# Kernel tuning notes

Measured on AMD Instinct MI355X. Metric: run time of the kernel, lower is better.

## Reference

```python
import jax, jax.numpy as jnp
import numpy as np

B, S, E, H = 4, 2048, 1024, 16
D = E // H  # head_dim = 64


def setup_inputs() -> dict:
    key = jax.random.key(0)
    ks = jax.random.split(key, 5)
    return {
        "hidden_states": jax.random.normal(ks[0], (B, S, E), dtype=jnp.float32),
        "c_attn_w": jax.random.normal(ks[1], (E, 3 * E), dtype=jnp.float32) * 0.02,
        "c_attn_b": jax.random.normal(ks[2], (3 * E,), dtype=jnp.float32) * 0.02,
        "c_proj_w": jax.random.normal(ks[3], (E, E), dtype=jnp.float32) * 0.02,
        "c_proj_b": jax.random.normal(ks[4], (E,), dtype=jnp.float32) * 0.02,
    }


def reference(hidden_states, c_attn_w, c_attn_b, c_proj_w, c_proj_b):
    b, s, e = hidden_states.shape
    # Conv1D c_attn: y = x @ W + b  -> qkv [b, s, 3E]
    qkv = hidden_states @ c_attn_w + c_attn_b
    q, k, v = jnp.split(qkv, 3, axis=-1)
    # split heads -> [b, H, s, D]
    def split_heads(t):
        return t.reshape(b, s, H, D).transpose(0, 2, 1, 3)
    q, k, v = split_heads(q), split_heads(k), split_heads(v)
    # QK^T scaled by sqrt(head_dim)
    scores = jnp.einsum("bhqd,bhkd->bhqk", q, k) / jnp.sqrt(
        jnp.asarray(D, dtype=q.dtype)
    )
    # causal mask (tril), masked positions get dtype min
    causal = jnp.tril(jnp.ones((s, s), dtype=bool))[None, None]
    mask_value = jnp.finfo(scores.dtype).min
    scores = jnp.where(causal, scores, mask_value)
    attn = jax.nn.softmax(scores, axis=-1)
    # attend to values, merge heads
    out = jnp.einsum("bhqk,bhkd->bhqd", attn, v)
    out = out.transpose(0, 2, 1, 3).reshape(b, s, e)
    # Conv1D c_proj
    return out @ c_proj_w + c_proj_b
```

## Files before the change

kernel.cpp:

```cpp
#include <hip/hip_runtime.h>
#include <hip/hip_bf16.h>
#include <cstdint>
#include <cstddef>

#define BB 4
#define SS 2048
#define EE 1024
#define HH 16
#define DD 64

typedef __attribute__((ext_vector_type(8))) short bf16x8;
typedef __attribute__((ext_vector_type(4))) float f32x4;

__device__ __forceinline__ short f2bf(float f) {
    union { float f; uint32_t u; } x; x.f = f;
    uint32_t r = (x.u + 0x7fffu + ((x.u >> 16) & 1u)) >> 16;
    return (short)r;
}
__device__ __forceinline__ short f2bf_fast(float f) {
    union { float f; uint32_t u; } x; x.f = f;
    return (short)((x.u + 0x8000u) >> 16);
}

__device__ __forceinline__ void gload16(const void* g, void* l) {
    __builtin_amdgcn_global_load_lds(
        (__attribute__((address_space(1))) uint32_t*)(uintptr_t)g,
        (__attribute__((address_space(3))) uint32_t*)(uint32_t)(uintptr_t)l,
        16, 0, 0);
}

#define WAIT_BARRIER(N)                                          \
    asm volatile("s_waitcnt vmcnt(" #N ")" ::: "memory");        \
    __builtin_amdgcn_s_barrier();                                \
    __builtin_amdgcn_sched_barrier(0);

template<int CTRL>
__device__ __forceinline__ float dppmove(float v) {
    return __int_as_float(__builtin_amdgcn_update_dpp(
        0, __float_as_int(v), CTRL, 0xf, 0xf, true));
}
#define ROW_REDUCE(vals, OP)                                             \
    _Pragma("unroll") for (int _r = 0; _r < 4; ++_r) {                   \
        vals[_r] = OP(vals[_r], dppmove<0xB1>(vals[_r]));                \
        vals[_r] = OP(vals[_r], dppmove<0x4E>(vals[_r]));                \
        vals[_r] = OP(vals[_r], dppmove<0x124>(vals[_r]));               \
        vals[_r] = OP(vals[_r], dppmove<0x128>(vals[_r]));               \
    }
__device__ __forceinline__ float opmax(float a, float b) { return fmaxf(a, b); }
__device__ __forceinline__ float opsum(float a, float b) { return a + b; }

__global__ void cast_kernel(const float* __restrict__ in, short* __restrict__ out, int n4) {
    int stride = gridDim.x * blockDim.x;
    for (int i = blockIdx.x * blockDim.x + threadIdx.x; i < n4; i += stride) {
        float4 v = reinterpret_cast<const float4*>(in)[i];
        short4 o;
        o.x = f2bf(v.x); o.y = f2bf(v.y); o.z = f2bf(v.z); o.w = f2bf(v.w);
        reinterpret_cast<short4*>(out)[i] = o;
    }
}

__global__ void transpose_cast_kernel(const float* __restrict__ in, short* __restrict__ out,
                                      int ncols, int nrows) {
    __shared__ float ts[32][33];
    const int t = threadIdx.x;
    const int r = t >> 3, c4 = (t & 7) * 4;
    const int n0 = blockIdx.x * 32, k0 = blockIdx.y * 32;
    float4 v = *reinterpret_cast<const float4*>(&in[(size_t)(k0 + r) * ncols + n0 + c4]);
    ts[c4 + 0][r] = v.x; ts[c4 + 1][r] = v.y; ts[c4 + 2][r] = v.z; ts[c4 + 3][r] = v.w;
    __syncthreads();
    short4 ov;
    ov.x = f2bf(ts[r][c4 + 0]); ov.y = f2bf(ts[r][c4 + 1]);
    ov.z = f2bf(ts[r][c4 + 2]); ov.w = f2bf(ts[r][c4 + 3]);
    *reinterpret_cast<short4*>(&out[(size_t)(n0 + r) * nrows + k0 + c4]) = ov;
}

__global__ __launch_bounds__(512, 2)
void gemm_qkv(const short* __restrict__ A, const short* __restrict__ Bt,
              const float* __restrict__ bias,
              short* __restrict__ Qo, short* __restrict__ Ko, short* __restrict__ Vo)
{
    __shared__ short As[3][4096];
    __shared__ short Bs[3][8192];
    const int tid  = threadIdx.x;
    const int lane = tid & 63, wid = tid >> 6;
    const int wr = wid >> 2, wc = wid & 3;
    const int l15 = lane & 15, lhi = lane >> 4;
    const int m0 = blockIdx.y * 128, n0 = blockIdx.x * 256;
    const int sr   = lane >> 2;
    const int scol = 8 * ((lane & 3) ^ ((lane >> 3) & 3));
    const int rdx  = (lhi ^ ((l15 >> 1) & 3)) << 4;

    f32x4 acc[4][4] = {};

#define QKV_STAGE(tt, bufi)                                                      \
    {                                                                            \
        const int kk = (tt) * 32;                                                \
        gload16(&A[(size_t)(m0 + wid * 16 + sr) * EE + kk + scol],               \
                (char*)&As[bufi][0] + wid * 1024);                               \
        gload16(&Bt[(size_t)(n0 + wid * 32 + sr) * EE + kk + scol],              \
                (char*)&Bs[bufi][0] + wid * 2048);                               \
        gload16(&Bt[(size_t)(n0 + wid * 32 + 16 + sr) * EE + kk + scol],         \
                (char*)&Bs[bufi][0] + wid * 2048 + 1024);                        \
    }

    QKV_STAGE(0, 0)
    QKV_STAGE(1, 1)
    WAIT_BARRIER(3)

    for (int kt = 0; kt < 32; ++kt) {
        const int cur = kt % 3;
        if (kt + 2 < 32) { const int nb = (kt + 2) % 3; QKV_STAGE(kt + 2, nb) }

        bf16x8 af[4], bfr[4];
        #pragma unroll
        for (int mm = 0; mm < 4; ++mm)
            af[mm] = *reinterpret_cast<const bf16x8*>(
                (const char*)&As[cur][0] + (wr * 64 + mm * 16 + l15) * 64 + rdx);
        #pragma unroll
        for (int nn = 0; nn < 4; ++nn)
            bfr[nn] = *reinterpret_cast<const bf16x8*>(
                (const char*)&Bs[cur][0] + (wc * 64 + nn * 16 + l15) * 64 + rdx);
        #pragma unroll
        for (int mm = 0; mm < 4; ++mm)
            #pragma unroll
            for (int nn = 0; nn < 4; ++nn)
                acc[mm][nn] = __builtin_amdgcn_mfma_f32_16x16x32_bf16(af[mm], bfr[nn], acc[mm][nn], 0, 0, 0);

        if (kt < 30)       { WAIT_BARRIER(3) }
        else if (kt == 30) { WAIT_BARRIER(0) }
    }
#undef QKV_STAGE

    const int part = n0 >> 10;
    #pragma unroll
    for (int mm = 0; mm < 4; ++mm) {
        #pragma unroll
        for (int nn = 0; nn < 4; ++nn) {
            const int gcol = n0 + wc * 64 + nn * 16 + l15;
            const float bv = bias[gcol];
            const int e = gcol & 1023;
            const int h = e >> 6, d = e & 63;
            const int grow0 = m0 + wr * 64 + mm * 16 + lhi * 4;
            const int bidx = grow0 >> 11;
            const int s0 = grow0 & 2047;
            const int bh = bidx * HH + h;
            if (part == 2) {
                short4 pk;
                pk.x = f2bf(acc[mm][nn][0] + bv);
                pk.y = f2bf(acc[mm][nn][1] + bv);
                pk.z = f2bf(acc[mm][nn][2] + bv);
                pk.w = f2bf(acc[mm][nn][3] + bv);
                *reinterpret_cast<short4*>(&Vo[((size_t)bh * DD + d) * SS + s0]) = pk;
            } else if (part == 0) {
                #pragma unroll
                for (int r = 0; r < 4; ++r)
                    Qo[((size_t)bh * SS + s0 + r) * DD + d] = f2bf((acc[mm][nn][r] + bv) * 0.18033688f);
            } else {
                #pragma unroll
                for (int r = 0; r < 4; ++r)
                    Ko[((size_t)bh * SS + s0 + r) * DD + d] = f2bf(acc[mm][nn][r] + bv);
            }
        }
    }
}

__global__ __launch_bounds__(256, 2)
void gemm_proj(const short* __restrict__ A, const short* __restrict__ Bt,
               const float* __restrict__ bias, float* __restrict__ Co)
{
    __shared__ short As[3][4096];
    __shared__ short Bs[3][4096];
    const int tid  = threadIdx.x;
    const int lane = tid & 63, wid = tid >> 6;
    const int wr = wid >> 1, wc = wid & 1;
    const int l15 = lane & 15, lhi = lane >> 4;
    const int m0 = blockIdx.y * 128, n0 = blockIdx.x * 128;
    const int sr   = lane >> 2;
    const int scol = 8 * ((lane & 3) ^ ((lane >> 3) & 3));
    const int rdx  = (lhi ^ ((l15 >> 1) & 3)) << 4;

    f32x4 acc[4][4] = {};

#define PROJ_STAGE(tt, bufi)                                                     \
    {                                                                            \
        const int kk = (tt) * 32;                                                \
        _Pragma("unroll")                                                        \
        for (int p = 0; p < 2; ++p) {                                            \
            const int c = wid * 2 + p;                                           \
            gload16(&A [(size_t)(m0 + c * 16 + sr) * EE + kk + scol],            \
                    (char*)&As[bufi][0] + c * 1024);                             \
            gload16(&Bt[(size_t)(n0 + c * 16 + sr) * EE + kk + scol],            \
                    (char*)&Bs[bufi][0] + c * 1024);                             \
        }                                                                        \
    }

    PROJ_STAGE(0, 0)
    PROJ_STAGE(1, 1)
    WAIT_BARRIER(4)

    for (int kt = 0; kt < 32; ++kt) {
        const int cur = kt % 3;
        if (kt + 2 < 32) { const int nb = (kt + 2) % 3; PROJ_STAGE(kt + 2, nb) }

        bf16x8 af[4], bfr[4];
        #pragma unroll
        for (int mm = 0; mm < 4; ++mm)
            af[mm] = *reinterpret_cast<const bf16x8*>(
                (const char*)&As[cur][0] + (wr * 64 + mm * 16 + l15) * 64 + rdx);
        #pragma unroll
        for (int nn = 0; nn < 4; ++nn)
            bfr[nn] = *reinterpret_cast<const bf16x8*>(
                (const char*)&Bs[cur][0] + (wc * 64 + nn * 16 + l15) * 64 + rdx);
        #pragma unroll
        for (int mm = 0; mm < 4; ++mm)
            #pragma unroll
            for (int nn = 0; nn < 4; ++nn)
                acc[mm][nn] = __builtin_amdgcn_mfma_f32_16x16x32_bf16(af[mm], bfr[nn], acc[mm][nn], 0, 0, 0);

        if (kt < 30)       { WAIT_BARRIER(4) }
        else if (kt == 30) { WAIT_BARRIER(0) }
    }
#undef PROJ_STAGE

    #pragma unroll
    for (int mm = 0; mm < 4; ++mm) {
        #pragma unroll
        for (int nn = 0; nn < 4; ++nn) {
            const int gcol = n0 + wc * 64 + nn * 16 + l15;
            const float bv = bias[gcol];
            #pragma unroll
            for (int r = 0; r < 4; ++r) {
                const int grow = m0 + wr * 64 + mm * 16 + lhi * 4 + r;
                Co[(size_t)grow * EE + gcol] = acc[mm][nn][r] + bv;
            }
        }
    }
}

__global__ __launch_bounds__(256, 4)
void attn_kernel(const short* __restrict__ Q, const short* __restrict__ K,
                 const short* __restrict__ Vt, short* __restrict__ CTX)
{
    __shared__ short Ks[4096];
    __shared__ short Vs[2][4096];
    __shared__ short Ps[4][1024];
    const int tid  = threadIdx.x;
    const int lane = tid & 63, wid = tid >> 6;
    const int l15 = lane & 15, lhi = lane >> 4;
    const int bid  = blockIdx.x;
    const int bh   = (bid & 7) * 8 + ((bid >> 3) & 7);
    const int pair = bid >> 6;
    const int b = bh >> 4, h = bh & 15;
    const size_t base = (size_t)bh * (SS * DD);
    const short* VtBase = Vt + (size_t)bh * (DD * SS);
    char* const pw = (char*)&Ps[wid][0];

    const int srow = lane >> 3;
    const int scol = 8 * ((lane & 7) ^ srow);

    for (int phase = 0; phase < 2; ++phase) {
        const int t = phase ? (31 - pair) : pair;
        const int q0 = t * 64;
        const int qbase = q0 + wid * 16;

        bf16x8 qa[2];
        qa[0] = *reinterpret_cast<const bf16x8*>(&Q[base + (size_t)(qbase + l15) * DD + lhi * 8]);
        qa[1] = *reinterpret_cast<const bf16x8*>(&Q[base + (size_t)(qbase + l15) * DD + 32 + lhi * 8]);

        f32x4 o[4] = {};
        float lrow[4] = {0.f, 0.f, 0.f, 0.f};

        #pragma unroll
        for (int p = 0; p < 2; ++p) {
            const int c = wid * 2 + p;
            gload16(&K     [base + (size_t)(c * 8 + srow) * DD + scol], (char*)Ks + c * 1024);
            gload16(&VtBase[(size_t)(c * 8 + srow) * SS + scol],        (char*)&Vs[0][0] + c * 1024);
        }
        __syncthreads();

        for (int kt = 0; kt <= t; ++kt) {
            const int cur = kt & 1;

            f32x4 sc[4];
            #pragma unroll
            for (int n = 0; n < 4; ++n) {
                const int row = n * 16 + l15;
                f32x4 cacc = {};
                #pragma unroll
                for (int ks = 0; ks < 2; ++ks) {
                    const int byteoff = (ks * 64 + lhi * 16) ^ ((l15 & 7) << 4);
                    bf16x8 kb = *reinterpret_cast<const bf16x8*>((const char*)Ks + row * 128 + byteoff);
                    cacc = __builtin_amdgcn_mfma_f32_16x16x32_bf16(qa[ks], kb, cacc, 0, 0, 0);
                }
                sc[n] = cacc;
            }

            __syncthreads();

            if (kt < t) {
                const int k1 = (kt + 1) * 64;
                #pragma unroll
                for (int p = 0; p < 2; ++p) {
                    const int c = wid * 2 + p;
                    gload16(&K     [base + (size_t)(k1 + c * 8 + srow) * DD + scol], (char*)Ks + c * 1024);
                    gload16(&VtBase[(size_t)(c * 8 + srow) * SS + k1 + scol], (char*)&Vs[cur ^ 1][0] + c * 1024);
                }
            }

            if (kt == t) {
                #pragma unroll
                for (int n = 0; n < 4; ++n) {
                    const int col = n * 16 + l15;
                    #pragma unroll
                    for (int r = 0; r < 4; ++r) {
                        const int qrow = wid * 16 + lhi * 4 + r;
                        if (col > qrow) sc[n][r] = -1e30f;
                    }
                }
            }
            #pragma unroll
            for (int n = 0; n < 4; ++n)
                #pragma unroll
                for (int r = 0; r < 4; ++r) sc[n][r] = __builtin_amdgcn_exp2f(sc[n][r]);
            #pragma unroll
            for (int n = 0; n < 4; ++n)
                #pragma unroll
                for (int r = 0; r < 4; ++r) {
                    const int q = lhi * 4 + r;
                    const int cb = (n * 32 + l15 * 2) ^ ((q & 7) << 4);
                    *reinterpret_cast<short*>(pw + q * 128 + cb) = f2bf_fast(sc[n][r]);
                }
            bf16x8 pa[2];
            #pragma unroll
            for (int ks = 0; ks < 2; ++ks)
                pa[ks] = *reinterpret_cast<const bf16x8*>(
                    pw + l15 * 128 + ((ks * 64 + lhi * 16) ^ ((l15 & 7) << 4)));
            #pragma unroll
            for (int dg = 0; dg < 4; ++dg) {
                const int row = dg * 16 + l15;
                #pragma unroll
                for (int ks = 0; ks < 2; ++ks) {
                    const int byteoff = (ks * 64 + lhi * 16) ^ ((l15 & 7) << 4);
                    bf16x8 vb = *reinterpret_cast<const bf16x8*>((const char*)&Vs[cur][0] + row * 128 + byteoff);
                    o[dg] = __builtin_amdgcn_mfma_f32_16x16x32_bf16(pa[ks], vb, o[dg], 0, 0, 0);
                }
            }
            float tsum[4];
            #pragma unroll
            for (int r = 0; r < 4; ++r)
                tsum[r] = (sc[0][r] + sc[1][r]) + (sc[2][r] + sc[3][r]);
            ROW_REDUCE(tsum, opsum)
            #pragma unroll
            for (int r = 0; r < 4; ++r) lrow[r] += tsum[r];

            __syncthreads();
        }

        #pragma unroll
        for (int dg = 0; dg < 4; ++dg)
            #pragma unroll
            for (int r = 0; r < 4; ++r) {
                int s = qbase + lhi * 4 + r;
                float val = o[dg][r] / lrow[r];
                CTX[(size_t)(b * SS + s) * EE + h * DD + dg * 16 + l15] = f2bf(val);
            }
    }
}

extern "C" void kernel_launch(void* const* d_in, const int* in_sizes, int n_in,
                              void* d_out, int out_size, void* d_ws, size_t ws_size,
                              hipStream_t stream) {
    const float* hs     = (const float*)d_in[0];
    const float* attn_w = (const float*)d_in[1];
    const float* attn_b = (const float*)d_in[2];
    const float* proj_w = (const float*)d_in[3];
    const float* proj_b = (const float*)d_in[4];
    float* out = (float*)d_out;

    char* ws = (char*)d_ws;
    short* Xb    = (short*)(ws + 0);
    short* WqkvT = (short*)(ws + 16777216);
    short* WprojT= (short*)(ws + 23068672);
    short* Qb    = (short*)(ws + 25165824);
    short* Kb    = (short*)(ws + 41943040);
    short* Vb    = (short*)(ws + 58720256);
    short* CTX   = Xb;

    cast_kernel<<<dim3(2048), dim3(256), 0, stream>>>(hs, Xb, (BB * SS * EE) / 4);
    transpose_cast_kernel<<<dim3(3 * EE / 32, EE / 32), dim3(256), 0, stream>>>(attn_w, WqkvT, 3 * EE, EE);
    transpose_cast_kernel<<<dim3(EE / 32, EE / 32), dim3(256), 0, stream>>>(proj_w, WprojT, EE, EE);

    gemm_qkv<<<dim3(3 * EE / 256, BB * SS / 128), dim3(512), 0, stream>>>(
        Xb, WqkvT, attn_b, Qb, Kb, Vb);

    attn_kernel<<<dim3(1024), dim3(256), 0, stream>>>(Qb, Kb, Vb, CTX);

    gemm_proj<<<dim3(EE / 128, BB * SS / 128), dim3(256), 0, stream>>>(
        CTX, WprojT, proj_b, out);
}
```

Before: 169.5 us.

## Rewrite QKV GEMM as 256x256 tile with 8-phase ping-pong pipeline

The QKV projection GEMM moves from a 128x256 tile with a K=32 triple buffer to a 256x256 tile with K=64 double-buffered chunks. Each iteration interleaves LDS fragment reads, the async global-to-LDS loads and MFMA groups across eight barrier-separated phases, and raises wave priority around the MFMA groups. The aim is more data reuse per tile and better overlap of loads with matrix math. In exchange it needs more accumulator registers (occupancy drops to 1 block per CU) and launches half as many blocks, which may leave CUs underused; the projection GEMM only gets its variables renamed.

```diff
diff --git a/kernel.cpp b/kernel.cpp
--- a/kernel.cpp
+++ b/kernel.cpp
@@ -28,11 +28,6 @@
         (__attribute__((address_space(3))) uint32_t*)(uint32_t)(uintptr_t)l,
         16, 0, 0);
 }
-
-#define WAIT_BARRIER(N)                                          \
-    asm volatile("s_waitcnt vmcnt(" #N ")" ::: "memory");        \
-    __builtin_amdgcn_s_barrier();                                \
-    __builtin_amdgcn_sched_barrier(0);
 
 template<int CTRL>
 __device__ __forceinline__ float dppmove(float v) {
@@ -74,73 +69,90 @@
     *reinterpret_cast<short4*>(&out[(size_t)(n0 + r) * nrows + k0 + c4]) = ov;
 }
 
-__global__ __launch_bounds__(512, 2)
+__global__ __launch_bounds__(512, 1)
 void gemm_qkv(const short* __restrict__ A, const short* __restrict__ Bt,
               const float* __restrict__ bias,
               short* __restrict__ Qo, short* __restrict__ Ko, short* __restrict__ Vo)
 {
-    __shared__ short As[3][4096];
-    __shared__ short Bs[3][8192];
+    __shared__ short As[2][4][4096];
+    __shared__ short Bs[2][4][4096];
     const int tid  = threadIdx.x;
     const int lane = tid & 63, wid = tid >> 6;
     const int wr = wid >> 2, wc = wid & 3;
     const int l15 = lane & 15, lhi = lane >> 4;
-    const int m0 = blockIdx.y * 128, n0 = blockIdx.x * 256;
-    const int sr   = lane >> 2;
-    const int scol = 8 * ((lane & 3) ^ ((lane >> 3) & 3));
-    const int rdx  = (lhi ^ ((l15 >> 1) & 3)) << 4;
-
-    f32x4 acc[4][4] = {};
-
-#define QKV_STAGE(tt, bufi)                                                      \
-    {                                                                            \
-        const int kk = (tt) * 32;                                                \
-        gload16(&A[(size_t)(m0 + wid * 16 + sr) * EE + kk + scol],               \
-                (char*)&As[bufi][0] + wid * 1024);                               \
-        gload16(&Bt[(size_t)(n0 + wid * 32 + sr) * EE + kk + scol],              \
-                (char*)&Bs[bufi][0] + wid * 2048);                               \
-        gload16(&Bt[(size_t)(n0 + wid * 32 + 16 + sr) * EE + kk + scol],         \
-                (char*)&Bs[bufi][0] + wid * 2048 + 1024);                        \
-    }
-
-    QKV_STAGE(0, 0)
-    QKV_STAGE(1, 1)
-    WAIT_BARRIER(3)
-
-    for (int kt = 0; kt < 32; ++kt) {
-        const int cur = kt % 3;
-        if (kt + 2 < 32) { const int nb = (kt + 2) % 3; QKV_STAGE(kt + 2, nb) }
-
-        bf16x8 af[4], bfr[4];
-        #pragma unroll
-        for (int mm = 0; mm < 4; ++mm)
-            af[mm] = *reinterpret_cast<const bf16x8*>(
-                (const char*)&As[cur][0] + (wr * 64 + mm * 16 + l15) * 64 + rdx);
-        #pragma unroll
-        for (int nn = 0; nn < 4; ++nn)
-            bfr[nn] = *reinterpret_cast<const bf16x8*>(
-                (const char*)&Bs[cur][0] + (wc * 64 + nn * 16 + l15) * 64 + rdx);
-        #pragma unroll
-        for (int mm = 0; mm < 4; ++mm)
-            #pragma unroll
-            for (int nn = 0; nn < 4; ++nn)
-                acc[mm][nn] = __builtin_amdgcn_mfma_f32_16x16x32_bf16(af[mm], bfr[nn], acc[mm][nn], 0, 0, 0);
-
-        if (kt < 30)       { WAIT_BARRIER(3) }
-        else if (kt == 30) { WAIT_BARRIER(0) }
-    }
-#undef QKV_STAGE
+    const int m0 = blockIdx.y * 256, n0 = blockIdx.x * 256;
+    const int srow = lane >> 3;
+    const int scol = 8 * ((lane & 7) ^ srow);
+    const int xorr = (l15 & 7) << 4;
+
+    f32x4 acc[8][4] = {};
+    bf16x8 af[4][2];
+    bf16x8 bfr[2][2][2];
+
+#define STGA(p, c0, c1, tt)                                                              \
+    gload16(&A[(size_t)(m0 + (c0)*64 + wid*8 + srow) * EE + (tt)*64 + scol],             \
+            (char*)&As[p][c0][0] + wid*1024);                                            \
+    gload16(&A[(size_t)(m0 + (c1)*64 + wid*8 + srow) * EE + (tt)*64 + scol],             \
+            (char*)&As[p][c1][0] + wid*1024);
+#define STGB(p, c0, c1, tt)                                                              \
+    gload16(&Bt[(size_t)(n0 + (c0)*64 + wid*8 + srow) * EE + (tt)*64 + scol],            \
+            (char*)&Bs[p][c0][0] + wid*1024);                                            \
+    gload16(&Bt[(size_t)(n0 + (c1)*64 + wid*8 + srow) * EE + (tt)*64 + scol],            \
+            (char*)&Bs[p][c1][0] + wid*1024);
+#define RDA(p, mq)                                                                       \
+    _Pragma("unroll") for (int mf = 0; mf < 4; ++mf)                                     \
+    _Pragma("unroll") for (int kh = 0; kh < 2; ++kh)                                     \
+        af[mf][kh] = *reinterpret_cast<const bf16x8*>((const char*)&As[p][wr*2+(mq)][0]  \
+            + (mf*16 + l15)*128 + ((kh*64 + lhi*16) ^ xorr));
+#define RDB(p, nq, st)                                                                   \
+    _Pragma("unroll") for (int nf = 0; nf < 2; ++nf)                                     \
+    _Pragma("unroll") for (int kh = 0; kh < 2; ++kh)                                     \
+        bfr[st][nf][kh] = *reinterpret_cast<const bf16x8*>((const char*)&Bs[p][wc][0]    \
+            + ((nq)*32 + nf*16 + l15)*128 + ((kh*64 + lhi*16) ^ xorr));
+#define MMA(mq, nq, st)                                                                  \
+    __builtin_amdgcn_s_setprio(1);                                                       \
+    _Pragma("unroll") for (int mf = 0; mf < 4; ++mf)                                     \
+    _Pragma("unroll") for (int nf = 0; nf < 2; ++nf)                                     \
+    _Pragma("unroll") for (int kh = 0; kh < 2; ++kh)                                     \
+        acc[(mq)*4+mf][(nq)*2+nf] = __builtin_amdgcn_mfma_f32_16x16x32_bf16(             \
+            af[mf][kh], bfr[st][nf][kh], acc[(mq)*4+mf][(nq)*2+nf], 0, 0, 0);            \
+    __builtin_amdgcn_s_setprio(0);
+#define BARS { __builtin_amdgcn_s_barrier(); __builtin_amdgcn_sched_barrier(0); }
+#define VMW(n) asm volatile("s_waitcnt vmcnt(" #n ")" ::: "memory");
+
+    STGA(0, 0, 2, 0) STGB(0, 0, 1, 0) STGB(0, 2, 3, 0) STGA(0, 1, 3, 0)
+    STGA(1, 0, 2, 1) STGB(1, 0, 1, 1) STGB(1, 2, 3, 1)
+    VMW(8) BARS
+
+    for (int i = 0; i < 8; ++i) {
+        const int tb  = 2*i + 1;
+        const int ta2 = (i < 7) ? 2*i + 2 : 15;
+        const int tb2 = (i < 7) ? 2*i + 3 : 15;
+        RDA(0,0) RDB(0,0,0) STGA(1,1,3,tb)  BARS MMA(0,0,0)         BARS
+        RDB(0,1,1)          STGA(0,0,2,ta2) BARS MMA(0,1,1) VMW(10) BARS
+        RDA(0,1)            STGB(0,0,1,ta2) BARS MMA(1,0,0)         BARS
+                            STGB(0,2,3,ta2) BARS MMA(1,1,1) VMW(8)  BARS
+        RDA(1,0) RDB(1,0,0) STGA(0,1,3,ta2) BARS MMA(0,0,0)         BARS
+        RDB(1,1,1)          STGA(1,0,2,tb2) BARS MMA(0,1,1) VMW(10) BARS
+        RDA(1,1)            STGB(1,0,1,tb2) BARS MMA(1,0,0)         BARS
+                            STGB(1,2,3,tb2) BARS MMA(1,1,1) VMW(8)  BARS
+    }
+#undef STGA
+#undef STGB
+#undef RDA
+#undef RDB
+#undef MMA
 
     const int part = n0 >> 10;
     #pragma unroll
-    for (int mm = 0; mm < 4; ++mm) {
+    for (int mm = 0; mm < 8; ++mm) {
         #pragma unroll
         for (int nn = 0; nn < 4; ++nn) {
             const int gcol = n0 + wc * 64 + nn * 16 + l15;
             const float bv = bias[gcol];
             const int e = gcol & 1023;
             const int h = e >> 6, d = e & 63;
-            const int grow0 = m0 + wr * 64 + mm * 16 + lhi * 4;
+            const int grow0 = m0 + wr * 128 + mm * 16 + lhi * 4;
             const int bidx = grow0 >> 11;
             const int s0 = grow0 & 2047;
             const int bh = bidx * HH + h;
@@ -196,29 +208,29 @@
 
     PROJ_STAGE(0, 0)
     PROJ_STAGE(1, 1)
-    WAIT_BARRIER(4)
+    VMW(4) BARS
 
     for (int kt = 0; kt < 32; ++kt) {
         const int cur = kt % 3;
         if (kt + 2 < 32) { const int nb = (kt + 2) % 3; PROJ_STAGE(kt + 2, nb) }
 
-        bf16x8 af[4], bfr[4];
+        bf16x8 af2[4], bf2[4];
         #pragma unroll
         for (int mm = 0; mm < 4; ++mm)
-            af[mm] = *reinterpret_cast<const bf16x8*>(
+            af2[mm] = *reinterpret_cast<const bf16x8*>(
                 (const char*)&As[cur][0] + (wr * 64 + mm * 16 + l15) * 64 + rdx);
         #pragma unroll
         for (int nn = 0; nn < 4; ++nn)
-            bfr[nn] = *reinterpret_cast<const bf16x8*>(
+            bf2[nn] = *reinterpret_cast<const bf16x8*>(
                 (const char*)&Bs[cur][0] + (wc * 64 + nn * 16 + l15) * 64 + rdx);
         #pragma unroll
         for (int mm = 0; mm < 4; ++mm)
             #pragma unroll
             for (int nn = 0; nn < 4; ++nn)
-                acc[mm][nn] = __builtin_amdgcn_mfma_f32_16x16x32_bf16(af[mm], bfr[nn], acc[mm][nn], 0, 0, 0);
-
-        if (kt < 30)       { WAIT_BARRIER(4) }
-        else if (kt == 30) { WAIT_BARRIER(0) }
+                acc[mm][nn] = __builtin_amdgcn_mfma_f32_16x16x32_bf16(af2[mm], bf2[nn], acc[mm][nn], 0, 0, 0);
+
+        if (kt < 30)       { VMW(4) BARS }
+        else if (kt == 30) { VMW(0) BARS }
     }
 #undef PROJ_STAGE
 
@@ -390,7 +402,7 @@
     transpose_cast_kernel<<<dim3(3 * EE / 32, EE / 32), dim3(256), 0, stream>>>(attn_w, WqkvT, 3 * EE, EE);
     transpose_cast_kernel<<<dim3(EE / 32, EE / 32), dim3(256), 0, stream>>>(proj_w, WprojT, EE, EE);
 
-    gemm_qkv<<<dim3(3 * EE / 256, BB * SS / 128), dim3(512), 0, stream>>>(
+    gemm_qkv<<<dim3(3 * EE / 256, BB * SS / 256), dim3(512), 0, stream>>>(
         Xb, WqkvT, attn_b, Qb, Kb, Vb);
 
     attn_kernel<<<dim3(1024), dim3(256), 0, stream>>>(Qb, Kb, Vb, CTX);
```

Measured after the change: 180.6 us. 1.07x slower.

## Enlarge attention query tile to 128 rows with 8 waves per block

Applied to the files above, without the earlier changes.

The attention kernel now runs 512-thread blocks, each covering 128 query rows (8 waves of 16 rows). Each K/V tile loaded into shared memory is therefore reused by twice as many query rows, which halves global K/V traffic per query and halves the block count. In exchange, causal masking is generalized to a per-wave check because the diagonal now spans two key tiles. Waves near the top of the tile do wasted masked work on the last key tile, and the larger blocks may lower occupancy.

```diff
diff --git a/kernel.cpp b/kernel.cpp
--- a/kernel.cpp
+++ b/kernel.cpp
@@ -202,20 +202,20 @@
         const int cur = kt % 3;
         if (kt + 2 < 32) { const int nb = (kt + 2) % 3; PROJ_STAGE(kt + 2, nb) }
 
-        bf16x8 af[4], bfr[4];
+        bf16x8 af2[4], bf2[4];
         #pragma unroll
         for (int mm = 0; mm < 4; ++mm)
-            af[mm] = *reinterpret_cast<const bf16x8*>(
+            af2[mm] = *reinterpret_cast<const bf16x8*>(
                 (const char*)&As[cur][0] + (wr * 64 + mm * 16 + l15) * 64 + rdx);
         #pragma unroll
         for (int nn = 0; nn < 4; ++nn)
-            bfr[nn] = *reinterpret_cast<const bf16x8*>(
+            bf2[nn] = *reinterpret_cast<const bf16x8*>(
                 (const char*)&Bs[cur][0] + (wc * 64 + nn * 16 + l15) * 64 + rdx);
         #pragma unroll
         for (int mm = 0; mm < 4; ++mm)
             #pragma unroll
             for (int nn = 0; nn < 4; ++nn)
-                acc[mm][nn] = __builtin_amdgcn_mfma_f32_16x16x32_bf16(af[mm], bfr[nn], acc[mm][nn], 0, 0, 0);
+                acc[mm][nn] = __builtin_amdgcn_mfma_f32_16x16x32_bf16(af2[mm], bf2[nn], acc[mm][nn], 0, 0, 0);
 
         if (kt < 30)       { WAIT_BARRIER(4) }
         else if (kt == 30) { WAIT_BARRIER(0) }
@@ -237,13 +237,13 @@
     }
 }
 
-__global__ __launch_bounds__(256, 4)
+__global__ __launch_bounds__(512, 2)
 void attn_kernel(const short* __restrict__ Q, const short* __restrict__ K,
                  const short* __restrict__ Vt, short* __restrict__ CTX)
 {
     __shared__ short Ks[4096];
     __shared__ short Vs[2][4096];
-    __shared__ short Ps[4][1024];
+    __shared__ short Ps[8][1024];
     const int tid  = threadIdx.x;
     const int lane = tid & 63, wid = tid >> 6;
     const int l15 = lane & 15, lhi = lane >> 4;
@@ -259,9 +259,10 @@
     const int scol = 8 * ((lane & 7) ^ srow);
 
     for (int phase = 0; phase < 2; ++phase) {
-        const int t = phase ? (31 - pair) : pair;
-        const int q0 = t * 64;
+        const int t = phase ? (15 - pair) : pair;
+        const int q0 = t * 128;
         const int qbase = q0 + wid * 16;
+        const int nkt = 2 * t + 2;
 
         bf16x8 qa[2];
         qa[0] = *reinterpret_cast<const bf16x8*>(&Q[base + (size_t)(qbase + l15) * DD + lhi * 8]);
@@ -270,16 +271,13 @@
         f32x4 o[4] = {};
         float lrow[4] = {0.f, 0.f, 0.f, 0.f};
 
-        #pragma unroll
-        for (int p = 0; p < 2; ++p) {
-            const int c = wid * 2 + p;
-            gload16(&K     [base + (size_t)(c * 8 + srow) * DD + scol], (char*)Ks + c * 1024);
-            gload16(&VtBase[(size_t)(c * 8 + srow) * SS + scol],        (char*)&Vs[0][0] + c * 1024);
-        }
+        gload16(&K     [base + (size_t)(wid * 8 + srow) * DD + scol], (char*)Ks + wid * 1024);
+        gload16(&VtBase[(size_t)(wid * 8 + srow) * SS + scol],        (char*)&Vs[0][0] + wid * 1024);
         __syncthreads();
 
-        for (int kt = 0; kt <= t; ++kt) {
+        for (int kt = 0; kt < nkt; ++kt) {
             const int cur = kt & 1;
+            const int k0 = kt * 64;
 
             f32x4 sc[4];
             #pragma unroll
@@ -297,23 +295,19 @@
 
             __syncthreads();
 
-            if (kt < t) {
-                const int k1 = (kt + 1) * 64;
-                #pragma unroll
-                for (int p = 0; p < 2; ++p) {
-                    const int c = wid * 2 + p;
-                    gload16(&K     [base + (size_t)(k1 + c * 8 + srow) * DD + scol], (char*)Ks + c * 1024);
-                    gload16(&VtBase[(size_t)(c * 8 + srow) * SS + k1 + scol], (char*)&Vs[cur ^ 1][0] + c * 1024);
-                }
-            }
-
-            if (kt == t) {
+            if (kt + 1 < nkt) {
+                const int k1 = k0 + 64;
+                gload16(&K     [base + (size_t)(k1 + wid * 8 + srow) * DD + scol], (char*)Ks + wid * 1024);
+                gload16(&VtBase[(size_t)(wid * 8 + srow) * SS + k1 + scol], (char*)&Vs[cur ^ 1][0] + wid * 1024);
+            }
+
+            if (k0 + 63 > qbase) {
                 #pragma unroll
                 for (int n = 0; n < 4; ++n) {
-                    const int col = n * 16 + l15;
+                    const int col = k0 + n * 16 + l15;
                     #pragma unroll
                     for (int r = 0; r < 4; ++r) {
-                        const int qrow = wid * 16 + lhi * 4 + r;
+                        const int qrow = qbase + lhi * 4 + r;
                         if (col > qrow) sc[n][r] = -1e30f;
                     }
                 }
@@ -393,7 +387,7 @@
     gemm_qkv<<<dim3(3 * EE / 256, BB * SS / 128), dim3(512), 0, stream>>>(
         Xb, WqkvT, attn_b, Qb, Kb, Vb);
 
-    attn_kernel<<<dim3(1024), dim3(256), 0, stream>>>(Qb, Kb, Vb, CTX);
+    attn_kernel<<<dim3(512), dim3(512), 0, stream>>>(Qb, Kb, Vb, CTX);
 
     gemm_proj<<<dim3(EE / 128, BB * SS / 128), dim3(256), 0, stream>>>(
         CTX, WprojT, proj_b, out);
```

Measured after the change: 167.8 us. About the same (-1.0%).
